# Kernel tuning notes

Hardware: AMD Instinct MI355X
Metric: run time of the kernel (lower is better)

## Reference

```python
import jax, jax.numpy as jnp
import numpy as np

SQRT3 = 1.7320508075688772
SQRT3_2 = 0.8660254037844386
SQRT3_3 = 0.5773502691896257

N_POINTS = 8388608
CAM_RINGS = 24      # hex camera rings -> 3*R^2+3*R+1 = 1801 pixels
KERNEL_RINGS = 1    # splat stencil rings -> 7 neighbor offsets
SIGMA = 0.5


def _build_sensor():
    """Precompute the static (eqx.field(static=True)) sensor geometry, faithfully
    reproducing _detect_hex_grid / _build_lookup_table / _hex_neighbor_offsets."""
    R = CAM_RINGS
    qs = [(q, r) for q in range(-R, R + 1) for r in range(-R, R + 1)
          if max(abs(q), abs(r), abs(q + r)) <= R]
    q = np.array([a for a, _ in qs], np.float64)
    r = np.array([b for _, b in qs], np.float64)
    centers = np.stack([SQRT3 * (q + r / 2.0), 1.5 * r], axis=1)  # pointy-top, size=1
    n = len(centers)
    # _detect_hex_grid
    diff = centers[:, None, :] - centers[None, :, :]
    dist_sq = (diff ** 2).sum(-1)
    np.fill_diagonal(dist_sq, np.inf)
    min_dist = np.sqrt(dist_sq.min())
    i, j = np.unravel_index(np.argmin(dist_sq), dist_sq.shape)
    vec = centers[i] - centers[j]
    rot = float(np.mod(np.arctan2(vec[1], vec[0]), np.pi / 3.0))
    offset = centers[np.argmin((centers ** 2).sum(1))]
    hex_size = float(min_dist / SQRT3)
    # _build_lookup_table
    xs = centers[:, 0] - offset[0]
    ys = centers[:, 1] - offset[1]
    c, s = np.cos(-rot), np.sin(-rot)
    xr = c * xs - s * ys
    yr = s * xs + c * ys
    qf = (SQRT3_3 * xr - yr / 3.0) / hex_size
    rf = 2.0 * yr / 3.0 / hex_size
    qi = np.round(qf).astype(np.int32)
    ri = np.round(rf).astype(np.int32)
    q_min, r_min = int(qi.min()), int(ri.min())
    table = np.full((int(qi.max()) - q_min + 1, int(ri.max()) - r_min + 1), -1, np.int32)
    table[qi - q_min, ri - r_min] = np.arange(n, dtype=np.int32)
    # _hex_neighbor_offsets
    K = KERNEL_RINGS
    offs = [(a, b) for a in range(-K, K + 1) for b in range(-K, K + 1)
            if max(abs(a), abs(b), abs(a + b)) <= K]
    nq = np.array([o[0] for o in offs], np.int32)
    nr = np.array([o[1] for o in offs], np.int32)
    ox = (hex_size * SQRT3 * (nq + nr / 2.0)).astype(np.float32)
    oy = (hex_size * 1.5 * nr).astype(np.float32)
    return dict(
        lookup_table=jnp.asarray(table),
        neighbor_q=jnp.asarray(nq), neighbor_r=jnp.asarray(nr),
        neighbor_ox=jnp.asarray(ox), neighbor_oy=jnp.asarray(oy),
        hex_size=hex_size, hex_inradius=hex_size * SQRT3_2,
        grid_rotation=rot, grid_offset=(float(offset[0]), float(offset[1])),
        q_min=q_min, r_min=r_min, n_pixels=n,
    )

SENSOR = _build_sensor()


def _axial_round(q, r):
    s = -q - r
    qi, ri, si = jnp.round(q), jnp.round(r), jnp.round(s)
    dq, dr, ds = jnp.abs(qi - q), jnp.abs(ri - r), jnp.abs(si - s)
    qi = jnp.where((dq > dr) & (dq > ds), -ri - si, qi)
    ri = jnp.where((dr > dq) & (dr > ds), -qi - si, ri)
    return qi, ri


def setup_inputs() -> dict:
    key = jax.random.key(0)
    k1, k2, k3 = jax.random.split(key, 3)
    # camera footprint half-extent ~ SQRT3*CAM_RINGS; sample mostly inside
    L = 0.6 * SQRT3 * CAM_RINGS
    x = jax.random.uniform(k1, (N_POINTS,), jnp.float32, -L, L)
    y = jax.random.uniform(k2, (N_POINTS,), jnp.float32, -L, L)
    values = jax.random.normal(k3, (N_POINTS,), jnp.float32)
    return {"x": x, "y": y, "values": values}


def reference(x, y, values):
    S = SENSOR
    hs = S["hex_size"]
    inr = S["hex_inradius"]
    # rotate into grid frame by -grid_rotation
    c = jnp.cos(-S["grid_rotation"]).astype(x.dtype) if False else np.float32(np.cos(-S["grid_rotation"]))
    s = np.float32(np.sin(-S["grid_rotation"]))
    xs = x - np.float32(S["grid_offset"][0])
    ys = y - np.float32(S["grid_offset"][1])
    x_g = c * xs - s * ys
    y_g = s * xs + c * ys
    # cartesian -> fractional axial -> nearest hex center
    q = (SQRT3_3 * x_g - y_g / 3.0) / hs
    r = 2.0 * y_g / 3.0 / hs
    q_base, r_base = _axial_round(q, r)
    base_x = hs * SQRT3 * (q_base + r_base / 2.0)
    base_y = hs * 1.5 * r_base
    dx = x_g - base_x
    dy = y_g - base_y
    # neighbor stencil: [P, 7]
    qi = q_base[:, None].astype(jnp.int32) + S["neighbor_q"]
    ri = r_base[:, None].astype(jnp.int32) + S["neighbor_r"]
    dist_x = dx[:, None] - S["neighbor_ox"]
    dist_y = dy[:, None] - S["neighbor_oy"]
    hex_dist = jnp.maximum(jnp.abs(dist_y),
                           SQRT3_2 * jnp.abs(dist_x) + 0.5 * jnp.abs(dist_y)) / inr
    weights = jnp.exp(-0.5 * (hex_dist / SIGMA) ** 2)
    weights = weights / weights.sum(axis=1, keepdims=True)
    # lookup-table gather with bounds masking
    tbl = S["lookup_table"]
    q_idx = qi - S["q_min"]
    r_idx = ri - S["r_min"]
    in_bounds = (q_idx >= 0) & (q_idx < tbl.shape[0]) & (r_idx >= 0) & (r_idx < tbl.shape[1])
    q_safe = jnp.clip(q_idx, 0, tbl.shape[0] - 1)
    r_safe = jnp.clip(r_idx, 0, tbl.shape[1] - 1)
    pixel_idx = tbl[q_safe, r_safe]
    valid = in_bounds & (pixel_idx >= 0)
    pixel_idx = jnp.where(valid, pixel_idx, 0)
    splatted = values[:, None] * weights * valid
    return jax.ops.segment_sum(splatted.reshape(-1), pixel_idx.reshape(-1),
                               num_segments=S["n_pixels"])
```

## Files before the change

kernel.cpp:

```cpp
#include <hip/hip_runtime.h>
#include <hip/hip_bf16.h>

#define NPIX 1801
#define NT   256
#define NB   2048

#define FXSCALE 1048576.0f
#define FXINV   (1.0f / 1048576.0f)

__device__ __forceinline__ int col_base(int q) {
    int a = q + 24;
    return (q <= 0) ? (a * 26 + ((a * (a - 1)) >> 1))
                    : (900 + 49 * q - ((q * (q - 1)) >> 1));
}

__device__ __forceinline__ bool in_hex(int q, int r) {
    return (unsigned)(q + 24) <= 48u && (unsigned)(r + 24) <= 48u &&
           (unsigned)(q + r + 24) <= 48u;
}

__global__ __launch_bounds__(NT) void hexsplat_kernel(
    const float* __restrict__ xs, const float* __restrict__ ys,
    const float* __restrict__ vs, unsigned int* __restrict__ acc, int n4)
{
    __shared__ unsigned int hist[NPIX];
    for (int i = threadIdx.x; i < NPIX; i += NT) hist[i] = 0u;
    __syncthreads();

    const float nox[7] = {-1.7320508075688772f, -0.8660254037844386f,
                          -0.8660254037844386f, 0.0f, 0.8660254037844386f,
                          0.8660254037844386f, 1.7320508075688772f};
    const float noy[7] = {0.0f, 1.5f, -1.5f, 0.0f, 1.5f, -1.5f, 0.0f};
    const int ncol[7] = {0, 0, 1, 1, 1, 2, 2};
    const int nrow[7] = {0, 1, -1, 0, 1, -1, 0};
    const int nq_[7]  = {-1, -1, 0, 0, 0, 1, 1};

    const int tid = blockIdx.x * NT + threadIdx.x;
    const int stride = NB * NT;
    const float4* x4 = (const float4*)xs;
    const float4* y4 = (const float4*)ys;
    const float4* v4 = (const float4*)vs;

    for (int i = tid; i < n4; i += stride) {
        float4 xq = x4[i];
        float4 yq = y4[i];
        float4 vq = v4[i];
        #pragma unroll
        for (int k = 0; k < 4; ++k) {
            float px = (&xq.x)[k];
            float py = (&yq.x)[k];
            float pv = (&vq.x)[k];

            float q = 0.5773502691896258f * px - 0.3333333333333333f * py;
            float r = 0.6666666666666666f * py;

            float sn = -q - r;
            float qi = rintf(q), ri = rintf(r), si = rintf(sn);
            float dq = fabsf(qi - q), dr = fabsf(ri - r), ds = fabsf(si - sn);
            if (dq > dr && dq > ds)      qi = -ri - si;
            else if (dr > dq && dr > ds) ri = -qi - si;

            int qb = (int)qi;
            int rb = (int)ri;

            float dx = px - 1.7320508075688772f * (qi + 0.5f * ri);
            float dy = py - 1.5f * ri;

            float w[7];
            float wsum = 0.0f;
            #pragma unroll
            for (int nn = 0; nn < 7; ++nn) {
                float dxn = dx - nox[nn];
                float dyn = dy - noy[nn];
                float ady = fabsf(dyn);
                float hd = fmaxf(ady, 0.8660254037844386f * fabsf(dxn) + 0.5f * ady)
                           * 1.1547005383792517f;
                float t = hd + hd;
                float wi = __expf(-0.5f * t * t);
                w[nn] = wi;
                wsum += wi;
            }
            float vinv = (pv / wsum) * FXSCALE;

            int b0 = col_base(qb - 1);
            int b1 = col_base(qb);
            int b2 = col_base(qb + 1);
            int cb[3] = {b0 + rb, b1 + rb, b2 + rb};

            bool interior = (unsigned)(qb + 23) <= 46u && (unsigned)(rb + 23) <= 46u &&
                            (unsigned)(qb + rb + 23) <= 46u;
            if (interior) {
                #pragma unroll
                for (int nn = 0; nn < 7; ++nn) {
                    int c = __float2int_rn(w[nn] * vinv);
                    atomicAdd(&hist[cb[ncol[nn]] + nrow[nn]], (unsigned int)c);
                }
            } else {
                #pragma unroll
                for (int nn = 0; nn < 7; ++nn) {
                    int qn = qb + nq_[nn];
                    int rn = rb + nrow[nn];
                    if (in_hex(qn, rn)) {
                        int c = __float2int_rn(w[nn] * vinv);
                        atomicAdd(&hist[cb[ncol[nn]] + nrow[nn]], (unsigned int)c);
                    }
                }
            }
        }
    }

    __syncthreads();
    for (int i = threadIdx.x; i < NPIX; i += NT) {
        atomicAdd(&acc[i], hist[i]);
    }
}

__global__ void finalize_kernel(const unsigned int* __restrict__ acc,
                                float* __restrict__ out)
{
    int i = blockIdx.x * blockDim.x + threadIdx.x;
    if (i < NPIX) out[i] = (float)(int)acc[i] * FXINV;
}

extern "C" void kernel_launch(void* const* d_in, const int* in_sizes, int n_in,
                              void* d_out, int out_size, void* d_ws, size_t ws_size,
                              hipStream_t stream) {
    const float* x = (const float*)d_in[0];
    const float* y = (const float*)d_in[1];
    const float* v = (const float*)d_in[2];
    float* out = (float*)d_out;
    unsigned int* acc = (unsigned int*)d_ws;
    int n = in_sizes[0];
    int n4 = n / 4;

    hipMemsetAsync(acc, 0, NPIX * sizeof(unsigned int), stream);
    hexsplat_kernel<<<NB, NT, 0, stream>>>(x, y, v, acc, n4);
    finalize_kernel<<<(NPIX + 255) / 256, 256, 0, stream>>>(acc, out);
}
```

Baseline: 153.1 us.

## Duplicate LDS histograms, slice global accumulators, and streamline weight math

Gives each block two shared histogram copies, chosen by thread parity, to reduce LDS atomic contention. The global flush now goes to up to 32 accumulator slices selected by block index, and the finalize kernel sums those slices. The Gaussian weights are rewritten with pre-scaled constants, a native exp2 and a native reciprocal, and interior addresses are computed in closed form without per-neighbor tables. The grid size is also doubled. Rounding changes from round-to-nearest to truncation, and the approximate rcp/exp2 can shift results slightly. Doubling the LDS footprint may also lower occupancy.

```diff
diff --git a/kernel.cpp b/kernel.cpp
--- a/kernel.cpp
+++ b/kernel.cpp
@@ -3,10 +3,25 @@
 
 #define NPIX 1801
 #define NT   256
-#define NB   2048
+#define NB   4096
+#define MAXSLICES 32
 
 #define FXSCALE 1048576.0f
 #define FXINV   (1.0f / 1048576.0f)
+#define KHD 1.9614249f
+#define KHX 1.6986438f
+
+#if __has_builtin(__builtin_amdgcn_exp2f)
+#define EXP2F(x) __builtin_amdgcn_exp2f(x)
+#else
+#define EXP2F(x) __expf((x) * 0.69314718f)
+#endif
+
+#if __has_builtin(__builtin_amdgcn_rcpf)
+#define RCPF(x) __builtin_amdgcn_rcpf(x)
+#else
+#define RCPF(x) (1.0f / (x))
+#endif
 
 __device__ __forceinline__ int col_base(int q) {
     int a = q + 24;
@@ -21,20 +36,15 @@
 
 __global__ __launch_bounds__(NT) void hexsplat_kernel(
     const float* __restrict__ xs, const float* __restrict__ ys,
-    const float* __restrict__ vs, unsigned int* __restrict__ acc, int n4)
+    const float* __restrict__ vs, unsigned int* __restrict__ acc,
+    int n4, int slice_mask)
 {
-    __shared__ unsigned int hist[NPIX];
-    for (int i = threadIdx.x; i < NPIX; i += NT) hist[i] = 0u;
+    __shared__ unsigned int hist[2 * NPIX];
+    #pragma unroll 4
+    for (int i = threadIdx.x; i < 2 * NPIX; i += NT) hist[i] = 0u;
     __syncthreads();
 
-    const float nox[7] = {-1.7320508075688772f, -0.8660254037844386f,
-                          -0.8660254037844386f, 0.0f, 0.8660254037844386f,
-                          0.8660254037844386f, 1.7320508075688772f};
-    const float noy[7] = {0.0f, 1.5f, -1.5f, 0.0f, 1.5f, -1.5f, 0.0f};
-    const int ncol[7] = {0, 0, 1, 1, 1, 2, 2};
-    const int nrow[7] = {0, 1, -1, 0, 1, -1, 0};
-    const int nq_[7]  = {-1, -1, 0, 0, 0, 1, 1};
-
+    const int pbase = (threadIdx.x & 1) ? NPIX : 0;
     const int tid = blockIdx.x * NT + threadIdx.x;
     const int stride = NB * NT;
     const float4* x4 = (const float4*)xs;
@@ -51,8 +61,8 @@
             float py = (&yq.x)[k];
             float pv = (&vq.x)[k];
 
-            float q = 0.5773502691896258f * px - 0.3333333333333333f * py;
-            float r = 0.6666666666666666f * py;
+            float q = fmaf(-0.33333334f, py, 0.57735027f * px);
+            float r = 0.66666669f * py;
 
             float sn = -q - r;
             float qi = rintf(q), ri = rintf(r), si = rintf(sn);
@@ -63,46 +73,61 @@
             int qb = (int)qi;
             int rb = (int)ri;
 
-            float dx = px - 1.7320508075688772f * (qi + 0.5f * ri);
-            float dy = py - 1.5f * ri;
+            float dx = fmaf(-1.7320508f, fmaf(0.5f, ri, qi), px);
+            float dy = fmaf(-1.5f, ri, py);
 
-            float w[7];
-            float wsum = 0.0f;
-            #pragma unroll
-            for (int nn = 0; nn < 7; ++nn) {
-                float dxn = dx - nox[nn];
-                float dyn = dy - noy[nn];
-                float ady = fabsf(dyn);
-                float hd = fmaxf(ady, 0.8660254037844386f * fabsf(dxn) + 0.5f * ady)
-                           * 1.1547005383792517f;
-                float t = hd + hd;
-                float wi = __expf(-0.5f * t * t);
-                w[nn] = wi;
-                wsum += wi;
-            }
-            float vinv = (pv / wsum) * FXSCALE;
+            float dm = dy - 1.5f,        dp = dy + 1.5f;
+            float em = dx - 0.8660254f,  ep = dx + 0.8660254f;
+            float eM = dx - 1.7320508f,  eP = dx + 1.7320508f;
+            float c0 = KHD * fabsf(dy), cm = KHD * fabsf(dm), cp = KHD * fabsf(dp);
+            float h0 = 0.5f * c0,       hm = 0.5f * cm,       hp = 0.5f * cp;
+            float u0 = fmaxf(c0, fmaf(KHX, fabsf(eP), h0));
+            float u1 = fmaxf(cm, fmaf(KHX, fabsf(ep), hm));
+            float u2 = fmaxf(cp, fmaf(KHX, fabsf(ep), hp));
+            float u3 = fmaxf(c0, fmaf(KHX, fabsf(dx), h0));
+            float u4 = fmaxf(cm, fmaf(KHX, fabsf(em), hm));
+            float u5 = fmaxf(cp, fmaf(KHX, fabsf(em), hp));
+            float u6 = fmaxf(c0, fmaf(KHX, fabsf(eM), h0));
+            float w0 = EXP2F(-(u0 * u0));
+            float w1 = EXP2F(-(u1 * u1));
+            float w2 = EXP2F(-(u2 * u2));
+            float w3 = EXP2F(-(u3 * u3));
+            float w4 = EXP2F(-(u4 * u4));
+            float w5 = EXP2F(-(u5 * u5));
+            float w6 = EXP2F(-(u6 * u6));
+            float wsum = ((w0 + w1) + (w2 + w3)) + ((w4 + w5) + w6);
+            float vinv = (pv * FXSCALE) * RCPF(wsum);
 
-            int b0 = col_base(qb - 1);
-            int b1 = col_base(qb);
-            int b2 = col_base(qb + 1);
-            int cb[3] = {b0 + rb, b1 + rb, b2 + rb};
-
-            bool interior = (unsigned)(qb + 23) <= 46u && (unsigned)(rb + 23) <= 46u &&
-                            (unsigned)(qb + rb + 23) <= 46u;
+            bool interior = ((unsigned)(qb + 23) <= 46u) &
+                            ((unsigned)(rb + 23) <= 46u) &
+                            ((unsigned)(qb + rb + 23) <= 46u);
             if (interior) {
-                #pragma unroll
-                for (int nn = 0; nn < 7; ++nn) {
-                    int c = __float2int_rn(w[nn] * vinv);
-                    atomicAdd(&hist[cb[ncol[nn]] + nrow[nn]], (unsigned int)c);
-                }
+                int m  = qb < 0 ? -qb : qb;
+                int t  = (m * (99 - m)) >> 1;
+                int b1 = 900 + rb + pbase + (qb < 0 ? -t : t);
+                int t2 = qb + qb;
+                int a0 = t2 - 1; a0 = a0 < 0 ? -a0 : a0;
+                int a2 = t2 + 1; a2 = a2 < 0 ? -a2 : a2;
+                int A0 = b1 - ((99 - a0) >> 1);
+                int A2 = b1 + ((99 - a2) >> 1);
+                atomicAdd(&hist[A0],     (unsigned int)(int)(w0 * vinv));
+                atomicAdd(&hist[A0 + 1], (unsigned int)(int)(w1 * vinv));
+                atomicAdd(&hist[b1 - 1], (unsigned int)(int)(w2 * vinv));
+                atomicAdd(&hist[b1],     (unsigned int)(int)(w3 * vinv));
+                atomicAdd(&hist[b1 + 1], (unsigned int)(int)(w4 * vinv));
+                atomicAdd(&hist[A2 - 1], (unsigned int)(int)(w5 * vinv));
+                atomicAdd(&hist[A2],     (unsigned int)(int)(w6 * vinv));
             } else {
+                const int nq_[7] = {-1, -1, 0, 0, 0, 1, 1};
+                const int nr_[7] = {0, 1, -1, 0, 1, -1, 0};
+                float warr[7] = {w0, w1, w2, w3, w4, w5, w6};
                 #pragma unroll
                 for (int nn = 0; nn < 7; ++nn) {
                     int qn = qb + nq_[nn];
-                    int rn = rb + nrow[nn];
+                    int rn = rb + nr_[nn];
                     if (in_hex(qn, rn)) {
-                        int c = __float2int_rn(w[nn] * vinv);
-                        atomicAdd(&hist[cb[ncol[nn]] + nrow[nn]], (unsigned int)c);
+                        atomicAdd(&hist[col_base(qn) + rn + pbase],
+                                  (unsigned int)(int)(warr[nn] * vinv));
                     }
                 }
             }
@@ -110,16 +135,21 @@
     }
 
     __syncthreads();
+    unsigned int* aslice = acc + (size_t)(blockIdx.x & slice_mask) * NPIX;
     for (int i = threadIdx.x; i < NPIX; i += NT) {
-        atomicAdd(&acc[i], hist[i]);
+        atomicAdd(&aslice[i], hist[i] + hist[i + NPIX]);
     }
 }
 
 __global__ void finalize_kernel(const unsigned int* __restrict__ acc,
-                                float* __restrict__ out)
+                                float* __restrict__ out, int nslices)
 {
     int i = blockIdx.x * blockDim.x + threadIdx.x;
-    if (i < NPIX) out[i] = (float)(int)acc[i] * FXINV;
+    if (i < NPIX) {
+        unsigned int s = 0;
+        for (int k = 0; k < nslices; ++k) s += acc[(size_t)k * NPIX + i];
+        out[i] = (float)(int)s * FXINV;
+    }
 }
 
 extern "C" void kernel_launch(void* const* d_in, const int* in_sizes, int n_in,
@@ -133,7 +163,12 @@
     int n = in_sizes[0];
     int n4 = n / 4;
 
-    hipMemsetAsync(acc, 0, NPIX * sizeof(unsigned int), stream);
-    hexsplat_kernel<<<NB, NT, 0, stream>>>(x, y, v, acc, n4);
-    finalize_kernel<<<(NPIX + 255) / 256, 256, 0, stream>>>(acc, out);
+    int nslices = 1;
+    while (nslices < MAXSLICES &&
+           (size_t)(nslices * 2) * NPIX * sizeof(unsigned int) <= ws_size)
+        nslices *= 2;
+
+    hipMemsetAsync(acc, 0, (size_t)nslices * NPIX * sizeof(unsigned int), stream);
+    hexsplat_kernel<<<NB, NT, 0, stream>>>(x, y, v, acc, n4, nslices - 1);
+    finalize_kernel<<<(NPIX + 255) / 256, 256, 0, stream>>>(acc, out, nslices);
 }
```

Result: faster. 137.2 us (-10.4%).
